# Optimization experiments

Hardware: AMD Instinct MI355X
Metric: run time of the kernel (lower is better)

Reference implementation:

```python
import jax, jax.numpy as jnp
import numpy as np

RANK = 256
ORDER = 3
B = 8192
NODES_PER = 9
NMAP = 5 ** 6          # 15625 dnn-key nodes
NDD = NMAP + 1         # + 1 device node
MDD = 2048             # edges into device node
POW5 = jnp.array([5**5, 5**4, 5**3, 5**2, 5, 1], dtype=jnp.int32)


def sage_gcn(x, src, dst, n, W, b):
    # DGL SAGEConv(aggregator='gcn'): h = fc((sum_in_neighbors + self) / (in_deg + 1))
    agg = jax.ops.segment_sum(x[src], dst, num_segments=n)
    deg = jax.ops.segment_sum(jnp.ones((src.shape[0],), x.dtype), dst, num_segments=n)
    h = (agg + x) / (deg + 1.0)[:, None]
    return h @ W + b


def layernorm(x, g, b, eps=1e-5):
    m = x.mean(-1, keepdims=True)
    v = ((x - m) ** 2).mean(-1, keepdims=True)
    return (x - m) * jax.lax.rsqrt(v + eps) * g + b


def setup_inputs() -> dict:
    key = jax.random.key(0)
    ks = jax.random.split(key, 10)
    rng = np.random.default_rng(0)
    # batched DNN graphs: B bidirectional 9-node chains
    base = np.arange(B, dtype=np.int32)[:, None] * NODES_PER
    s = (base + np.arange(NODES_PER - 1, dtype=np.int32)[None, :]).ravel()
    d = s + 1
    edge_src = jnp.asarray(np.concatenate([s, d]))
    edge_dst = jnp.asarray(np.concatenate([d, s]))
    # unique key tuples (base-5 digits of unique dnn indices)
    key_idx = rng.choice(NMAP, size=B, replace=False).astype(np.int32)
    digits = np.stack([(key_idx // 5 ** (5 - j)) % 5 for j in range(6)], axis=1)
    key_ids = jnp.asarray(digits, dtype=jnp.int32)
    features = jax.random.randint(ks[0], (B, NODES_PER), 0, 6, dtype=jnp.int32)
    dd_src = jnp.asarray(rng.choice(NMAP, size=MDD, replace=False).astype(np.int32))

    r = RANK
    def gn(k, shape, scale=0.02):
        return jax.random.normal(k, shape, jnp.float32) * scale

    return dict(
        features=features, key_ids=key_ids,
        edge_src=edge_src, edge_dst=edge_dst, dd_src=dd_src,
        emb=gn(ks[1], (6, r)),
        sage_W=gn(ks[2], (ORDER, r, r)), sage_b=jnp.zeros((ORDER, r)),
        ln_g=jnp.ones((ORDER, r)), ln_b=jnp.zeros((ORDER, r)),
        dd_W=gn(ks[3], (r, r)), dd_b=jnp.zeros((r,)),
        norm_g=jnp.ones((r,)), norm_b=jnp.zeros((r,)),
        info_W=gn(ks[4], (5, r)), info_b=jnp.zeros((r,)),
        aug_data=gn(ks[5], (1, 5), 1.0),
        pred_W1=gn(ks[6], (2 * r, r)), pred_b1=jnp.zeros((r,)),
        pred_W2=gn(ks[7], (r, 1)), pred_b2=jnp.zeros((1,)),
    )


def reference(features, key_ids, edge_src, edge_dst, dd_src,
              emb, sage_W, sage_b, ln_g, ln_b,
              dd_W, dd_b, norm_g, norm_b,
              info_W, info_b, aug_data,
              pred_W1, pred_b1, pred_W2, pred_b2):
    n = B * NODES_PER
    # GraphReader: embed + ORDER x (SAGEConv-gcn -> LayerNorm -> ReLU)
    feats = emb[features].reshape(n, RANK)
    for i in range(ORDER):
        feats = sage_gcn(feats, edge_src, edge_dst, n, sage_W[i], sage_b[i])
        feats = jax.nn.relu(layernorm(feats, ln_g[i], ln_b[i]))
    # first node of each 9-node sub-graph
    graph_embeds = feats.reshape(B, NODES_PER, RANK)[:, 0]  # [B, r]

    # scatter graph embeddings into the dnn-device graph node features
    key_idx = (key_ids * POW5).sum(axis=1)  # base-5 index from 6-tuple
    dd = jnp.zeros((NDD, RANK), feats.dtype).at[key_idx].set(graph_embeds)
    info = aug_data @ info_W + info_b  # [1, r]
    dd = dd.at[NDD - 1].set(info[0])

    # SAGEConv-gcn on the dnn-device graph (all edges point at the device node)
    dd_dst = jnp.full_like(dd_src, NDD - 1)
    dd = sage_gcn(dd, dd_src, dd_dst, NDD, dd_W, dd_b)
    dd = jax.nn.relu(layernorm(dd, norm_g, norm_b))

    info_embeds = jnp.broadcast_to(dd[-1], (B, RANK))
    embeds = jnp.concatenate([graph_embeds, info_embeds], axis=1)  # [B, 2r]
    h = jax.nn.relu(embeds @ pred_W1 + pred_b1)
    return h @ pred_W2 + pred_b2  # [B, 1]
```

## Files before the change

kernel.cpp:

```cpp
#include <hip/hip_runtime.h>

#define RANK 256
#define NB 8192
#define NMAP 15625

typedef unsigned short ushort_t;
typedef short  mfma_ab __attribute__((ext_vector_type(8)));
typedef float  f32x4   __attribute__((ext_vector_type(4)));

#define GEH_OFF   0
#define GEL_OFF   4194304
#define WTH_OFF   8388608
#define WTL_OFF   8912896
#define INV_OFF   9437184
#define PARTS_OFF 9499712
#define C2_OFF    9630784

#define DD_BLOCKS 128

__device__ __forceinline__ float b2f(ushort_t u) {
    return __uint_as_float(((unsigned)u) << 16);
}
__device__ __forceinline__ ushort_t f2b(float f) {
    unsigned u = __float_as_uint(f);
    return (ushort_t)((u + 0x7FFFu + ((u >> 16) & 1u)) >> 16);
}

__device__ __forceinline__ f32x4 mfma_bf16(mfma_ab a, mfma_ab b, f32x4 c) {
#if defined(__gfx950__)
    return __builtin_amdgcn_mfma_f32_16x16x32_bf16(a, b, c, 0, 0, 0);
#else
    (void)a; (void)b;
    return c;
#endif
}

__device__ __forceinline__ float sten1(float x, float up, float dn, int R) {
    int j = R % 9;
    float fu = (j != 0) ? 1.f : 0.f;
    float fd = (j != 8) ? 1.f : 0.f;
    float sc = (fu + fd > 1.5f) ? (1.f / 3.f) : 0.5f;
    return (x + fu * up + fd * dn) * sc;
}

__global__ void k_init_inv(int* inv) {
    int i = blockIdx.x * 256 + threadIdx.x;
    if (i < NMAP) inv[i] = -1;
}

__global__ void k_scatter(const int* key_ids, int* inv) {
    int b = blockIdx.x * 256 + threadIdx.x;
    const int* kp = key_ids + b * 6;
    int k = kp[0]*3125 + kp[1]*625 + kp[2]*125 + kp[3]*25 + kp[4]*5 + kp[5];
    inv[k] = b;
}

__global__ void k_prep_w(const float* __restrict__ sageW,
                         const float* __restrict__ predW1,
                         ushort_t* __restrict__ WTh,
                         ushort_t* __restrict__ WTl)
{
    const int id = blockIdx.x;
    const int mat = id >> 4, tile = id & 15;
    const int tr = tile >> 2, tc = tile & 3;
    const float* src = (mat < 3) ? (sageW + mat * 65536) : predW1;
    ushort_t* dh = WTh + mat * 65536;
    ushort_t* dl = WTl + mat * 65536;
    __shared__ float t[64][65];
    const int tid = threadIdx.x;
    const int c = tid & 63, r0 = tid >> 6;
    #pragma unroll
    for (int i = 0; i < 16; ++i) {
        int r = r0 + i * 4;
        t[r][c] = src[(tr*64 + r) * 256 + tc*64 + c];
    }
    __syncthreads();
    #pragma unroll
    for (int i = 0; i < 16; ++i) {
        int r = r0 + i * 4;
        float f = t[c][r];
        ushort_t h = f2b(f);
        dh[(tc*64 + r) * 256 + tr*64 + c] = h;
        dl[(tc*64 + r) * 256 + tr*64 + c] = f2b(f - b2f(h));
    }
}

#define GR_G 5
#define GR_ROWS 45
#define GR_RPAD 48
#define AP 264

#define LN_PART(ACC0, ACC1, MT)                                                \
    _Pragma("unroll")                                                          \
    for (int q = 0; q < 4; ++q) {                                              \
        ACC0[q] += bias0; ACC1[q] += bias1;                                    \
        float s_  = ACC0[q] + ACC1[q];                                         \
        float ss_ = ACC0[q] * ACC0[q] + ACC1[q] * ACC1[q];                     \
        _Pragma("unroll")                                                      \
        for (int mask = 1; mask <= 8; mask <<= 1) {                            \
            s_  += __shfl_xor(s_, mask, 64);                                   \
            ss_ += __shfl_xor(ss_, mask, 64);                                  \
        }                                                                      \
        const int prow_ = (MT) * 16 + q4 * 4 + q;                              \
        if (l15 == 0 && prow_ < GR_ROWS)                                       \
            sPart[prow_][wid] = make_float2(s_, ss_);                          \
    }

#define LN_WRITE(ACC0, ACC1, MT)                                               \
    _Pragma("unroll")                                                          \
    for (int q = 0; q < 4; ++q) {                                              \
        const int row_ = (MT) * 16 + q4 * 4 + q;                               \
        if (row_ < nreal) {                                                    \
            const float2 mr_ = sMV[row_];                                      \
            float v0_ = (ACC0[q] - mr_.x) * mr_.y * gv0 + bv0;                 \
            float v1_ = (ACC1[q] - mr_.x) * mr_.y * gv1 + bv1;                 \
            v0_ = fmaxf(v0_, 0.f); v1_ = fmaxf(v1_, 0.f);                      \
            const ushort_t h0_ = f2b(v0_), h1_ = f2b(v1_);                     \
            const ushort_t lo0_ = f2b(v0_ - b2f(h0_));                         \
            const ushort_t lo1_ = f2b(v1_ - b2f(h1_));                         \
            if (L < 2) {                                                       \
                sXh[row_ * AP + colb + l15]      = h0_;                        \
                sXl[row_ * AP + colb + l15]      = lo0_;                       \
                sXh[row_ * AP + colb + 16 + l15] = h1_;                        \
                sXl[row_ * AP + colb + 16 + l15] = lo1_;                       \
            } else if ((row_ % 9) == 0) {                                      \
                const int gi_ = row_ / 9;                                      \
                GEh[(b0 + gi_) * RANK + colb + l15]      = h0_;                \
                GEl[(b0 + gi_) * RANK + colb + l15]      = lo0_;               \
                GEh[(b0 + gi_) * RANK + colb + 16 + l15] = h1_;                \
                GEl[(b0 + gi_) * RANK + colb + 16 + l15] = lo1_;               \
            }                                                                  \
        }                                                                      \
    }

#define STENCIL_COL(V0, V1, V2)                                                \
    {                                                                          \
        float ui0 = __shfl(V0[3], lane - 16), di0 = __shfl(V0[0], lane + 16);  \
        float ui1 = __shfl(V1[3], lane - 16), di1 = __shfl(V1[0], lane + 16);  \
        float ui2 = __shfl(V2[3], lane - 16), di2 = __shfl(V2[0], lane + 16);  \
        float xu1 = __shfl(V0[3], l15 + 48);       \
        float xu2 = __shfl(V1[3], l15 + 48);       \
        float xd0 = __shfl(V1[0], l15);           \
        float xd1 = __shfl(V2[0], l15);           \
        const int rb0 = q4 * 4, rb1 = 16 + q4 * 4, rb2 = 32 + q4 * 4;          \
        float u0 = (q4 == 0) ? 0.f : ui0;                                      \
        float d0 = (q4 == 3) ? xd0 : di0;                                      \
        float u1 = (q4 == 0) ? xu1 : ui1;                                      \
        float d1 = (q4 == 3) ? xd1 : di1;                                      \
        float u2 = (q4 == 0) ? xu2 : ui2;                                      \
        float d2 = (q4 == 3) ? 0.f : di2;                                      \
        float z00 = sten1(V0[0], u0,    V0[1], rb0 + 0);                       \
        float z01 = sten1(V0[1], V0[0], V0[2], rb0 + 1);                       \
        float z02 = sten1(V0[2], V0[1], V0[3], rb0 + 2);                       \
        float z03 = sten1(V0[3], V0[2], d0,    rb0 + 3);                       \
        float z10 = sten1(V1[0], u1,    V1[1], rb1 + 0);                       \
        float z11 = sten1(V1[1], V1[0], V1[2], rb1 + 1);                       \
        float z12 = sten1(V1[2], V1[1], V1[3], rb1 + 2);                       \
        float z13 = sten1(V1[3], V1[2], d1,    rb1 + 3);                       \
        float z20 = sten1(V2[0], u2,    V2[1], rb2 + 0);                       \
        float z21 = sten1(V2[1], V2[0], V2[2], rb2 + 1);                       \
        float z22 = sten1(V2[2], V2[1], V2[3], rb2 + 2);                       \
        float z23 = sten1(V2[3], V2[2], d2,    rb2 + 3);                       \
        V0[0] = z00; V0[1] = z01; V0[2] = z02; V0[3] = z03;                    \
        V1[0] = z10; V1[1] = z11; V1[2] = z12; V1[3] = z13;                    \
        V2[0] = z20; V2[1] = z21; V2[2] = z22; V2[3] = z23;                    \
    }

__global__ __launch_bounds__(512, 4) void k_graph_reader(
    const int* __restrict__ features,
    const float* __restrict__ emb,
    const ushort_t* __restrict__ WTh,
    const ushort_t* __restrict__ WTl,
    const float* __restrict__ sageB,
    const float* __restrict__ lnG,
    const float* __restrict__ lnB,
    ushort_t* __restrict__ GEh,
    ushort_t* __restrict__ GEl)
{
    __shared__ __align__(16) ushort_t sXh[GR_RPAD * AP];
    __shared__ __align__(16) ushort_t sXl[GR_RPAD * AP];
    __shared__ float2 sPart[GR_ROWS][8];
    __shared__ float2 sMV[GR_ROWS];
    __shared__ int sFeat[GR_ROWS];

    const int tid  = threadIdx.x;
    const int wid  = tid >> 6;
    const int lane = tid & 63;
    const int q4   = lane >> 4;
    const int l15  = lane & 15;
    const int colb = wid * 32;

    const int b0    = blockIdx.x * GR_G;
    const int ngr   = min(GR_G, NB - b0);
    const int nreal = ngr * 9;

    if (tid < GR_ROWS) sFeat[tid] = (tid < nreal) ? features[b0 * 9 + tid] : 0;
    __syncthreads();

    #pragma unroll
    for (int it = 0; it < 6; ++it) {
        int t = tid + it * 512;
        int row = t >> 6, c4 = t & 63;
        float4 v = make_float4(0.f, 0.f, 0.f, 0.f);
        if (row < nreal)
            v = *(const float4*)(emb + sFeat[row] * RANK + c4 * 4);
        ushort_t h0 = f2b(v.x), h1 = f2b(v.y), h2 = f2b(v.z), h3 = f2b(v.w);
        ushort_t l0 = f2b(v.x - b2f(h0)), l1 = f2b(v.y - b2f(h1));
        ushort_t l2 = f2b(v.z - b2f(h2)), l3 = f2b(v.w - b2f(h3));
        *(uint2*)(sXh + row * AP + c4 * 4) =
            make_uint2((unsigned)h0 | ((unsigned)h1 << 16),
                       (unsigned)h2 | ((unsigned)h3 << 16));
        *(uint2*)(sXl + row * AP + c4 * 4) =
            make_uint2((unsigned)l0 | ((unsigned)l1 << 16),
                       (unsigned)l2 | ((unsigned)l3 << 16));
    }

    const f32x4 vzero = {0.f, 0.f, 0.f, 0.f};

    for (int L = 0; L < 3; ++L) {
        __syncthreads();

        f32x4 a00 = vzero, a01 = vzero;
        f32x4 a10 = vzero, a11 = vzero;
        f32x4 a20 = vzero, a21 = vzero;
        const ushort_t* bh = WTh + L * 65536 + (colb + l15) * RANK + q4 * 8;
        const ushort_t* bl = WTl + L * 65536 + (colb + l15) * RANK + q4 * 8;
        #pragma unroll
        for (int ks = 0; ks < 8; ++ks) {
            mfma_ab B0h = *(const mfma_ab*)(bh + ks * 32);
            mfma_ab B0l = *(const mfma_ab*)(bl + ks * 32);
            mfma_ab B1h = *(const mfma_ab*)(bh + 16 * RANK + ks * 32);
            mfma_ab B1l = *(const mfma_ab*)(bl + 16 * RANK + ks * 32);
            const int ab = l15 * AP + ks * 32 + q4 * 8;

            mfma_ab Ah = *(const mfma_ab*)(sXh + ab);
            mfma_ab Al = *(const mfma_ab*)(sXl + ab);
            a00 = mfma_bf16(Ah, B0h, a00);
            a00 = mfma_bf16(Al, B0h, a00);
            a00 = mfma_bf16(Ah, B0l, a00);
            a01 = mfma_bf16(Ah, B1h, a01);
            a01 = mfma_bf16(Al, B1h, a01);
            a01 = mfma_bf16(Ah, B1l, a01);

            Ah = *(const mfma_ab*)(sXh + ab + 16 * AP);
            Al = *(const mfma_ab*)(sXl + ab + 16 * AP);
            a10 = mfma_bf16(Ah, B0h, a10);
            a10 = mfma_bf16(Al, B0h, a10);
            a10 = mfma_bf16(Ah, B0l, a10);
            a11 = mfma_bf16(Ah, B1h, a11);
            a11 = mfma_bf16(Al, B1h, a11);
            a11 = mfma_bf16(Ah, B1l, a11);

            Ah = *(const mfma_ab*)(sXh + ab + 32 * AP);
            Al = *(const mfma_ab*)(sXl + ab + 32 * AP);
            a20 = mfma_bf16(Ah, B0h, a20);
            a20 = mfma_bf16(Al, B0h, a20);
            a20 = mfma_bf16(Ah, B0l, a20);
            a21 = mfma_bf16(Ah, B1h, a21);
            a21 = mfma_bf16(Al, B1h, a21);
            a21 = mfma_bf16(Ah, B1l, a21);
        }

        STENCIL_COL(a00, a10, a20)
        STENCIL_COL(a01, a11, a21)

        float bias0, bias1, gv0, gv1, bv0, bv1;
        {
            int col0 = colb + l15, col1 = colb + 16 + l15;
            bias0 = sageB[L * RANK + col0]; bias1 = sageB[L * RANK + col1];
            gv0   = lnG[L * RANK + col0];   gv1   = lnG[L * RANK + col1];
            bv0   = lnB[L * RANK + col0];   bv1   = lnB[L * RANK + col1];
        }

        LN_PART(a00, a01, 0)
        LN_PART(a10, a11, 1)
        LN_PART(a20, a21, 2)
        __syncthreads();

        if (tid < GR_ROWS) {
            float s = 0.f, q = 0.f;
            #pragma unroll
            for (int w = 0; w < 8; ++w) { float2 p = sPart[tid][w]; s += p.x; q += p.y; }
            float m = s * (1.0f / 256.0f);
            float var = q * (1.0f / 256.0f) - m * m;
            if (var < 0.f) var = 0.f;
            sMV[tid] = make_float2(m, rsqrtf(var + 1e-5f));
        }
        __syncthreads();

        LN_WRITE(a00, a01, 0)
        LN_WRITE(a10, a11, 1)
        LN_WRITE(a20, a21, 2)
    }
}

__global__ void k_dd_agg(const int* __restrict__ dd_src,
                         const int* __restrict__ inv,
                         const ushort_t* __restrict__ GEh,
                         const ushort_t* __restrict__ GEl,
                         float* __restrict__ parts)
{
    const int c  = threadIdx.x;
    const int e0 = blockIdx.x * (2048 / DD_BLOCKS);
    float s = 0.f;
    for (int e = e0; e < e0 + (2048 / DD_BLOCKS); ++e) {
        int b = inv[dd_src[e]];
        if (b >= 0) s += b2f(GEh[b * RANK + c]) + b2f(GEl[b * RANK + c]);
    }
    parts[blockIdx.x * RANK + c] = s;
}

__global__ void k_device(const float* __restrict__ parts,
                         const float* __restrict__ aug,
                         const float* __restrict__ infoW,
                         const float* __restrict__ infoB,
                         const float* __restrict__ ddW,
                         const float* __restrict__ ddB,
                         const float* __restrict__ normG,
                         const float* __restrict__ normB,
                         const float* __restrict__ predW1,
                         const float* __restrict__ predB1,
                         float* __restrict__ c2)
{
    __shared__ float sh[RANK];
    __shared__ float sdev[RANK];
    __shared__ float sred[RANK];
    const int n = threadIdx.x;

    float agg = 0.f;
    for (int p = 0; p < DD_BLOCKS; ++p) agg += parts[p * RANK + n];
    float info = infoB[n];
    for (int j = 0; j < 5; ++j) info += aug[j] * infoW[j * RANK + n];
    sh[n] = (agg + info) * (1.0f / 2049.0f);
    __syncthreads();

    float y = ddB[n];
    for (int k = 0; k < RANK; ++k) y += sh[k] * ddW[k * RANK + n];

    sred[n] = y; __syncthreads();
    for (int off = 128; off > 0; off >>= 1) {
        if (n < off) sred[n] += sred[n + off];
        __syncthreads();
    }
    float s = sred[0]; __syncthreads();
    sred[n] = y * y; __syncthreads();
    for (int off = 128; off > 0; off >>= 1) {
        if (n < off) sred[n] += sred[n + off];
        __syncthreads();
    }
    float q = sred[0]; __syncthreads();

    float m = s * (1.0f / 256.0f);
    float var = q * (1.0f / 256.0f) - m * m;
    if (var < 0.f) var = 0.f;
    float rs = rsqrtf(var + 1e-5f);
    float dev = (y - m) * rs * normG[n] + normB[n];
    if (dev < 0.f) dev = 0.f;
    sdev[n] = dev;
    __syncthreads();

    float o = predB1[n];
    for (int k = 0; k < RANK; ++k) o += sdev[k] * predW1[(RANK + k) * RANK + n];
    c2[n] = o;
}

#define PRED_MFMA3(ACC, AH, AL, BH, BL)                                        \
    ACC = mfma_bf16(AH, BH, ACC);                                              \
    ACC = mfma_bf16(AL, BH, ACC);                                              \
    ACC = mfma_bf16(AH, BL, ACC);

#define PRED_N(NT, C0, C1)                                                     \
    {                                                                          \
        mfma_ab Bh_ = *(const mfma_ab*)(bh + (NT) * 16 * RANK + ks * 32);      \
        mfma_ab Bl_ = *(const mfma_ab*)(bl + (NT) * 16 * RANK + ks * 32);      \
        PRED_MFMA3(C0, A0h, A0l, Bh_, Bl_)                                     \
        PRED_MFMA3(C1, A1h, A1l, Bh_, Bl_)                                     \
    }

#define PRED_EPI(NT, C0, C1)                                                   \
    {                                                                          \
        const int col_ = colb + (NT) * 16 + l15;                               \
        const float c2v_ = c2[col_], w2v_ = predW2[col_];                      \
        op00 += fmaxf(C0[0] + c2v_, 0.f) * w2v_;                               \
        op01 += fmaxf(C0[1] + c2v_, 0.f) * w2v_;                               \
        op02 += fmaxf(C0[2] + c2v_, 0.f) * w2v_;                               \
        op03 += fmaxf(C0[3] + c2v_, 0.f) * w2v_;                               \
        op10 += fmaxf(C1[0] + c2v_, 0.f) * w2v_;                               \
        op11 += fmaxf(C1[1] + c2v_, 0.f) * w2v_;                               \
        op12 += fmaxf(C1[2] + c2v_, 0.f) * w2v_;                               \
        op13 += fmaxf(C1[3] + c2v_, 0.f) * w2v_;                               \
    }

__global__ __launch_bounds__(128, 4) void k_pred(
    const ushort_t* __restrict__ GEh,
    const ushort_t* __restrict__ GEl,
    const ushort_t* __restrict__ W1h,
    const ushort_t* __restrict__ W1l,
    const float* __restrict__ c2,
    const float* __restrict__ predW2,
    const float* __restrict__ predB2,
    float* __restrict__ out)
{
    __shared__ float sO[2][32];
    const int tid = threadIdx.x;
    const int wid = tid >> 6;
    const int lane = tid & 63;
    const int q4 = lane >> 4, l15 = lane & 15;
    const int colb = wid * 128;
    const int m0 = blockIdx.x * 32;

    const f32x4 vzero = {0.f, 0.f, 0.f, 0.f};
    f32x4 c00 = vzero, c01 = vzero, c02 = vzero, c03 = vzero;
    f32x4 c04 = vzero, c05 = vzero, c06 = vzero, c07 = vzero;
    f32x4 c10 = vzero, c11 = vzero, c12 = vzero, c13 = vzero;
    f32x4 c14 = vzero, c15 = vzero, c16 = vzero, c17 = vzero;

    const ushort_t* ah0 = GEh + (m0 + l15) * RANK + q4 * 8;
    const ushort_t* al0 = GEl + (m0 + l15) * RANK + q4 * 8;
    const ushort_t* ah1 = ah0 + 16 * RANK;
    const ushort_t* al1 = al0 + 16 * RANK;
    const ushort_t* bh = W1h + (colb + l15) * RANK + q4 * 8;
    const ushort_t* bl = W1l + (colb + l15) * RANK + q4 * 8;

    #pragma unroll
    for (int ks = 0; ks < 8; ++ks) {
        mfma_ab A0h = *(const mfma_ab*)(ah0 + ks * 32);
        mfma_ab A0l = *(const mfma_ab*)(al0 + ks * 32);
        mfma_ab A1h = *(const mfma_ab*)(ah1 + ks * 32);
        mfma_ab A1l = *(const mfma_ab*)(al1 + ks * 32);
        PRED_N(0, c00, c10) PRED_N(1, c01, c11)
        PRED_N(2, c02, c12) PRED_N(3, c03, c13)
        PRED_N(4, c04, c14) PRED_N(5, c05, c15)
        PRED_N(6, c06, c16) PRED_N(7, c07, c17)
    }

    float op00 = 0.f, op01 = 0.f, op02 = 0.f, op03 = 0.f;
    float op10 = 0.f, op11 = 0.f, op12 = 0.f, op13 = 0.f;
    PRED_EPI(0, c00, c10) PRED_EPI(1, c01, c11)
    PRED_EPI(2, c02, c12) PRED_EPI(3, c03, c13)
    PRED_EPI(4, c04, c14) PRED_EPI(5, c05, c15)
    PRED_EPI(6, c06, c16) PRED_EPI(7, c07, c17)

    #pragma unroll
    for (int mask = 1; mask <= 8; mask <<= 1) {
        op00 += __shfl_xor(op00, mask, 64); op01 += __shfl_xor(op01, mask, 64);
        op02 += __shfl_xor(op02, mask, 64); op03 += __shfl_xor(op03, mask, 64);
        op10 += __shfl_xor(op10, mask, 64); op11 += __shfl_xor(op11, mask, 64);
        op12 += __shfl_xor(op12, mask, 64); op13 += __shfl_xor(op13, mask, 64);
    }
    if (l15 == 0) {
        sO[wid][q4 * 4 + 0] = op00; sO[wid][q4 * 4 + 1] = op01;
        sO[wid][q4 * 4 + 2] = op02; sO[wid][q4 * 4 + 3] = op03;
        sO[wid][16 + q4 * 4 + 0] = op10; sO[wid][16 + q4 * 4 + 1] = op11;
        sO[wid][16 + q4 * 4 + 2] = op12; sO[wid][16 + q4 * 4 + 3] = op13;
    }
    __syncthreads();
    if (tid < 32) out[m0 + tid] = sO[0][tid] + sO[1][tid] + predB2[0];
}

extern "C" void kernel_launch(void* const* d_in, const int* in_sizes, int n_in,
                              void* d_out, int out_size, void* d_ws, size_t ws_size,
                              hipStream_t stream) {
    const int* features  = (const int*)d_in[0];
    const int* key_ids   = (const int*)d_in[1];
    const int* dd_src    = (const int*)d_in[4];
    const float* emb     = (const float*)d_in[5];
    const float* sageW   = (const float*)d_in[6];
    const float* sageB   = (const float*)d_in[7];
    const float* lnG     = (const float*)d_in[8];
    const float* lnB     = (const float*)d_in[9];
    const float* ddW     = (const float*)d_in[10];
    const float* ddB     = (const float*)d_in[11];
    const float* normG   = (const float*)d_in[12];
    const float* normB   = (const float*)d_in[13];
    const float* infoW   = (const float*)d_in[14];
    const float* infoB   = (const float*)d_in[15];
    const float* aug     = (const float*)d_in[16];
    const float* predW1  = (const float*)d_in[17];
    const float* predB1  = (const float*)d_in[18];
    const float* predW2  = (const float*)d_in[19];
    const float* predB2  = (const float*)d_in[20];

    char* ws = (char*)d_ws;
    ushort_t* GEh   = (ushort_t*)(ws + GEH_OFF);
    ushort_t* GEl   = (ushort_t*)(ws + GEL_OFF);
    ushort_t* WTh   = (ushort_t*)(ws + WTH_OFF);
    ushort_t* WTl   = (ushort_t*)(ws + WTL_OFF);
    int*      inv   = (int*)(ws + INV_OFF);
    float*    parts = (float*)(ws + PARTS_OFF);
    float*    c2    = (float*)(ws + C2_OFF);
    float*    outp  = (float*)d_out;

    k_init_inv<<<62, 256, 0, stream>>>(inv);
    k_scatter<<<32, 256, 0, stream>>>(key_ids, inv);
    k_prep_w<<<64, 256, 0, stream>>>(sageW, predW1, WTh, WTl);
    k_graph_reader<<<(NB + GR_G - 1) / GR_G, 512, 0, stream>>>(
        features, emb, WTh, WTl, sageB, lnG, lnB, GEh, GEl);
    k_dd_agg<<<DD_BLOCKS, 256, 0, stream>>>(dd_src, inv, GEh, GEl, parts);
    k_device<<<1, 256, 0, stream>>>(parts, aug, infoW, infoB, ddW, ddB,
                                    normG, normB, predW1, predB1, c2);
    k_pred<<<NB / 32, 128, 0, stream>>>(GEh, GEl, WTh + 3 * 65536, WTl + 3 * 65536,
                                        c2, predW2, predB2, outp);
}
```

Before: 416.4 us.

## Split graph-reader columns across 16 waves with 1024-thread blocks

The graph reader kernel now launches 1024 threads (16 waves) per block. Each wave owns 16 output columns instead of 32, which halves per-wave accumulators, B-fragment loads and MFMA count. LayerNorm partial sums are reduced over 16 waves, and the embedding load loop is adjusted to match. The aim is more latency hiding and lower register pressure per wave, at the cost of more LDS re-reads of the A operand per block and bigger barriers.

```diff
diff --git a/kernel.cpp b/kernel.cpp
--- a/kernel.cpp
+++ b/kernel.cpp
@@ -90,12 +90,12 @@
 #define GR_RPAD 48
 #define AP 264
 
-#define LN_PART(ACC0, ACC1, MT)                                                \
+#define LN_PART1(ACC, MT)                                                      \
     _Pragma("unroll")                                                          \
     for (int q = 0; q < 4; ++q) {                                              \
-        ACC0[q] += bias0; ACC1[q] += bias1;                                    \
-        float s_  = ACC0[q] + ACC1[q];                                         \
-        float ss_ = ACC0[q] * ACC0[q] + ACC1[q] * ACC1[q];                     \
+        ACC[q] += bias0;                                                       \
+        float s_  = ACC[q];                                                    \
+        float ss_ = ACC[q] * ACC[q];                                           \
         _Pragma("unroll")                                                      \
         for (int mask = 1; mask <= 8; mask <<= 1) {                            \
             s_  += __shfl_xor(s_, mask, 64);                                   \
@@ -106,29 +106,23 @@
             sPart[prow_][wid] = make_float2(s_, ss_);                          \
     }
 
-#define LN_WRITE(ACC0, ACC1, MT)                                               \
+#define LN_WRITE1(ACC, MT)                                                     \
     _Pragma("unroll")                                                          \
     for (int q = 0; q < 4; ++q) {                                              \
         const int row_ = (MT) * 16 + q4 * 4 + q;                               \
         if (row_ < nreal) {                                                    \
             const float2 mr_ = sMV[row_];                                      \
-            float v0_ = (ACC0[q] - mr_.x) * mr_.y * gv0 + bv0;                 \
-            float v1_ = (ACC1[q] - mr_.x) * mr_.y * gv1 + bv1;                 \
-            v0_ = fmaxf(v0_, 0.f); v1_ = fmaxf(v1_, 0.f);                      \
-            const ushort_t h0_ = f2b(v0_), h1_ = f2b(v1_);                     \
+            float v0_ = (ACC[q] - mr_.x) * mr_.y * gv0 + bv0;                  \
+            v0_ = fmaxf(v0_, 0.f);                                             \
+            const ushort_t h0_ = f2b(v0_);                                     \
             const ushort_t lo0_ = f2b(v0_ - b2f(h0_));                         \
-            const ushort_t lo1_ = f2b(v1_ - b2f(h1_));                         \
             if (L < 2) {                                                       \
-                sXh[row_ * AP + colb + l15]      = h0_;                        \
-                sXl[row_ * AP + colb + l15]      = lo0_;                       \
-                sXh[row_ * AP + colb + 16 + l15] = h1_;                        \
-                sXl[row_ * AP + colb + 16 + l15] = lo1_;                       \
+                sXh[row_ * AP + colb + l15] = h0_;                             \
+                sXl[row_ * AP + colb + l15] = lo0_;                            \
             } else if ((row_ % 9) == 0) {                                      \
                 const int gi_ = row_ / 9;                                      \
-                GEh[(b0 + gi_) * RANK + colb + l15]      = h0_;                \
-                GEl[(b0 + gi_) * RANK + colb + l15]      = lo0_;               \
-                GEh[(b0 + gi_) * RANK + colb + 16 + l15] = h1_;                \
-                GEl[(b0 + gi_) * RANK + colb + 16 + l15] = lo1_;               \
+                GEh[(b0 + gi_) * RANK + colb + l15] = h0_;                     \
+                GEl[(b0 + gi_) * RANK + colb + l15] = lo0_;                    \
             }                                                                  \
         }                                                                      \
     }
@@ -166,7 +160,7 @@
         V2[0] = z20; V2[1] = z21; V2[2] = z22; V2[3] = z23;                    \
     }
 
-__global__ __launch_bounds__(512, 4) void k_graph_reader(
+__global__ __launch_bounds__(1024, 8) void k_graph_reader(
     const int* __restrict__ features,
     const float* __restrict__ emb,
     const ushort_t* __restrict__ WTh,
@@ -179,7 +173,7 @@
 {
     __shared__ __align__(16) ushort_t sXh[GR_RPAD * AP];
     __shared__ __align__(16) ushort_t sXl[GR_RPAD * AP];
-    __shared__ float2 sPart[GR_ROWS][8];
+    __shared__ float2 sPart[GR_ROWS][16];
     __shared__ float2 sMV[GR_ROWS];
     __shared__ int sFeat[GR_ROWS];
 
@@ -188,7 +182,7 @@
     const int lane = tid & 63;
     const int q4   = lane >> 4;
     const int l15  = lane & 15;
-    const int colb = wid * 32;
+    const int colb = wid * 16;
 
     const int b0    = blockIdx.x * GR_G;
     const int ngr   = min(GR_G, NB - b0);
@@ -198,8 +192,8 @@
     __syncthreads();
 
     #pragma unroll
-    for (int it = 0; it < 6; ++it) {
-        int t = tid + it * 512;
+    for (int it = 0; it < 3; ++it) {
+        int t = tid + it * 1024;
         int row = t >> 6, c4 = t & 63;
         float4 v = make_float4(0.f, 0.f, 0.f, 0.f);
         if (row < nreal)
@@ -220,67 +214,53 @@
     for (int L = 0; L < 3; ++L) {
         __syncthreads();
 
-        f32x4 a00 = vzero, a01 = vzero;
-        f32x4 a10 = vzero, a11 = vzero;
-        f32x4 a20 = vzero, a21 = vzero;
+        f32x4 a0 = vzero, a1 = vzero, a2 = vzero;
         const ushort_t* bh = WTh + L * 65536 + (colb + l15) * RANK + q4 * 8;
         const ushort_t* bl = WTl + L * 65536 + (colb + l15) * RANK + q4 * 8;
         #pragma unroll
         for (int ks = 0; ks < 8; ++ks) {
-            mfma_ab B0h = *(const mfma_ab*)(bh + ks * 32);
-            mfma_ab B0l = *(const mfma_ab*)(bl + ks * 32);
-            mfma_ab B1h = *(const mfma_ab*)(bh + 16 * RANK + ks * 32);
-            mfma_ab B1l = *(const mfma_ab*)(bl + 16 * RANK + ks * 32);
+            mfma_ab Bh = *(const mfma_ab*)(bh + ks * 32);
+            mfma_ab Bl = *(const mfma_ab*)(bl + ks * 32);
             const int ab = l15 * AP + ks * 32 + q4 * 8;
 
             mfma_ab Ah = *(const mfma_ab*)(sXh + ab);
             mfma_ab Al = *(const mfma_ab*)(sXl + ab);
-            a00 = mfma_bf16(Ah, B0h, a00);
-            a00 = mfma_bf16(Al, B0h, a00);
-            a00 = mfma_bf16(Ah, B0l, a00);
-            a01 = mfma_bf16(Ah, B1h, a01);
-            a01 = mfma_bf16(Al, B1h, a01);
-            a01 = mfma_bf16(Ah, B1l, a01);
+            a0 = mfma_bf16(Ah, Bh, a0);
+            a0 = mfma_bf16(Al, Bh, a0);
+            a0 = mfma_bf16(Ah, Bl, a0);
 
             Ah = *(const mfma_ab*)(sXh + ab + 16 * AP);
             Al = *(const mfma_ab*)(sXl + ab + 16 * AP);
-            a10 = mfma_bf16(Ah, B0h, a10);
-            a10 = mfma_bf16(Al, B0h, a10);
-            a10 = mfma_bf16(Ah, B0l, a10);
-            a11 = mfma_bf16(Ah, B1h, a11);
-            a11 = mfma_bf16(Al, B1h, a11);
-            a11 = mfma_bf16(Ah, B1l, a11);
+            a1 = mfma_bf16(Ah, Bh, a1);
+            a1 = mfma_bf16(Al, Bh, a1);
+            a1 = mfma_bf16(Ah, Bl, a1);
 
             Ah = *(const mfma_ab*)(sXh + ab + 32 * AP);
             Al = *(const mfma_ab*)(sXl + ab + 32 * AP);
-            a20 = mfma_bf16(Ah, B0h, a20);
-            a20 = mfma_bf16(Al, B0h, a20);
-            a20 = mfma_bf16(Ah, B0l, a20);
-            a21 = mfma_bf16(Ah, B1h, a21);
-            a21 = mfma_bf16(Al, B1h, a21);
-            a21 = mfma_bf16(Ah, B1l, a21);
+            a2 = mfma_bf16(Ah, Bh, a2);
+            a2 = mfma_bf16(Al, Bh, a2);
+            a2 = mfma_bf16(Ah, Bl, a2);
         }
 
-        STENCIL_COL(a00, a10, a20)
-        STENCIL_COL(a01, a11, a21)
-
-        float bias0, bias1, gv0, gv1, bv0, bv1;
+        STENCIL_COL(a0, a1, a2)
+
+        float bias0, gv0, bv0;
         {
-            int col0 = colb + l15, col1 = colb + 16 + l15;
-            bias0 = sageB[L * RANK + col0]; bias1 = sageB[L * RANK + col1];
-            gv0   = lnG[L * RANK + col0];   gv1   = lnG[L * RANK + col1];
-            bv0   = lnB[L * RANK + col0];   bv1   = lnB[L * RANK + col1];
+            int col0 = colb + l15;
+            bias0 = sageB[L * RANK + col0];
+            gv0   = lnG[L * RANK + col0];
+            bv0   = lnB[L * RANK + col0];
         }
 
-        LN_PART(a00, a01, 0)
-        LN_PART(a10, a11, 1)
-        LN_PART(a20, a21, 2)
+        LN_PART1(a0, 0)
+        LN_PART1(a1, 1)
+        LN_PART1(a2, 2)
         __syncthreads();
 
         if (tid < GR_ROWS) {
             float s = 0.f, q = 0.f;
             #pragma unroll
-            for (int w = 0; w < 8; ++w) { float2 p = sPart[tid][w]; s += p.x; q += p.y; }
+            for (int w = 0; w < 16; ++w) { float2 p = sPart[tid][w]; s += p.x; q += p.y; }
             float m = s * (1.0f / 256.0f);
             float var = q * (1.0f / 256.0f) - m * m;
             if (var < 0.f) var = 0.f;
@@ -288,9 +268,9 @@
         }
         __syncthreads();
 
-        LN_WRITE(a00, a01, 0)
-        LN_WRITE(a10, a11, 1)
-        LN_WRITE(a20, a21, 2)
+        LN_WRITE1(a0, 0)
+        LN_WRITE1(a1, 1)
+        LN_WRITE1(a2, 2)
     }
 }
 
@@ -494,7 +474,7 @@
     k_init_inv<<<62, 256, 0, stream>>>(inv);
     k_scatter<<<32, 256, 0, stream>>>(key_ids, inv);
     k_prep_w<<<64, 256, 0, stream>>>(sageW, predW1, WTh, WTl);
-    k_graph_reader<<<(NB + GR_G - 1) / GR_G, 512, 0, stream>>>(
+    k_graph_reader<<<(NB + GR_G - 1) / GR_G, 1024, 0, stream>>>(
         features, emb, WTh, WTl, sageB, lnG, lnB, GEh, GEl);
     k_dd_agg<<<DD_BLOCKS, 256, 0, stream>>>(dd_src, inv, GEh, GEl, parts);
     k_device<<<1, 256, 0, stream>>>(parts, aug, infoW, infoB, ddW, ddB,
```

After: 491.3 us. 1.18x slower.
